# Optimization experiments

Measured on AMD Instinct MI355X. Metric: run time of the kernel, lower is better.

The kernel has to match this reference:

```python
import jax, jax.numpy as jnp
import numpy as np

B, N = 8, 2048
DIN, DH, DE = 32, 64, 64
R = 3          # number_relations
L = 3          # num_layers -> 1 first + 1 block + 1 last
PRED_IN = DH * (L - 1) + DE  # concat: 64*2 + 64 = 192
EPS_BN = 1e-5
EPS_NORM = 1e-12


def setup_inputs() -> dict:
    key = jax.random.key(0)
    ks = jax.random.split(key, 12)
    x = jax.random.normal(ks[0], (B, N, DIN), jnp.float32)
    # relation labels in {0..R}; 0 = no edge, 1..R = relation type
    relation = jax.random.randint(ks[1], (B, N, N), 0, R + 1).astype(jnp.int32)
    # adjacency is the 0/1 edge indicator (float), as the torch code treats it
    adj = (relation > 0).astype(jnp.float32)
    s = 0.05
    w_first = jax.random.normal(ks[2], (R, DIN, DH), jnp.float32) * s
    b_first = jnp.zeros((DH,), jnp.float32)
    w_block = jax.random.normal(ks[3], (R, DH, DH), jnp.float32) * s
    b_block = jnp.zeros((DH,), jnp.float32)
    w_last = jax.random.normal(ks[4], (R, DH, DE), jnp.float32) * s
    b_last = jnp.zeros((DE,), jnp.float32)
    w_map = jax.random.normal(ks[5], (PRED_IN, DE), jnp.float32) * s
    b_map = jnp.zeros((DE,), jnp.float32)
    return {"x": x, "relation": relation, "adj": adj,
            "w_first": w_first, "b_first": b_first,
            "w_block": w_block, "b_block": b_block,
            "w_last": w_last, "b_last": b_last,
            "w_map": w_map, "b_map": b_map}


def _graph_conv(x, rel, W, b):
    # rel: [B,N,N] (int labels or float adjacency); W: [R, din, dout]
    y = jnp.zeros((x.shape[0], x.shape[1], W.shape[2]), x.dtype)
    for i in range(R):  # fixed, small relation count
        mask = (rel == (i + 1)).astype(x.dtype)            # [B,N,N]
        h = jnp.einsum('bij,bjd->bid', mask, x)            # masked aggregation
        y = y + jnp.einsum('bid,de->bie', h, W[i])
    y = y + b
    # F.normalize(p=2, dim=2): v / max(||v||, eps)
    nrm = jnp.sqrt(jnp.sum(y * y, axis=2, keepdims=True))
    return y / jnp.maximum(nrm, EPS_NORM)


def _apply_bn(x):
    # fresh BatchNorm1d(N) in training mode, affine weight=1/bias=0:
    # normalize over (batch, feature) per node index, biased variance
    mean = jnp.mean(x, axis=(0, 2), keepdims=True)
    var = jnp.mean(jnp.square(x - mean), axis=(0, 2), keepdims=True)
    return (x - mean) * jax.lax.rsqrt(var + EPS_BN)


def reference(x, relation, adj, w_first, b_first, w_block, b_block,
              w_last, b_last, w_map, b_map):
    # conv_first uses `relation`
    h = _apply_bn(jax.nn.relu(_graph_conv(x, relation, w_first, b_first)))
    out_all = [jnp.max(h, axis=1)]
    # conv_block and conv_last are (faithfully) called with `adj` as relation
    h = _apply_bn(jax.nn.relu(_graph_conv(h, adj, w_block, b_block)))
    out_all.append(jnp.max(h, axis=1))
    h = _graph_conv(h, adj, w_last, b_last)
    out_all.append(jnp.max(h, axis=1))
    output = jnp.concatenate(out_all, axis=1)        # [B, PRED_IN]
    ypred = output @ w_map + b_map                   # map_model Linear
    return (output, ypred)
```

## Files before the change

### kernel.cpp

```cpp
#include <hip/hip_runtime.h>


#define NN 2048
#define PLANE_W 1048576L

typedef short short8 __attribute__((ext_vector_type(8)));
typedef float floatx4 __attribute__((ext_vector_type(4)));

__device__ __forceinline__ unsigned short f2bf(float x) {
  unsigned u = __float_as_uint(x);
  u += 0x7FFFu + ((u >> 16) & 1u);
  return (unsigned short)(u >> 16);
}

__device__ void dev_xw_first(char* smemc, int u, int tid,
                             const float* __restrict__ x,
                             const float* __restrict__ w,
                             unsigned short* __restrict__ xws) {
  float* xs = (float*)smemc;
  float* wsh = (float*)(smemc + 64 * 33 * 4);
  const int jc = u & 31, b = (u >> 5) & 7, r = u >> 8;
  const int j0 = jc * 64;
  for (int idx = tid; idx < 64 * 32; idx += 256) {
    int row = idx >> 5, f = idx & 31;
    xs[row * 33 + f] = x[((long)b * NN + j0 + row) * 32 + f];
    wsh[idx] = w[r * 2048 + idx];
  }
  __syncthreads();
  const int j = tid & 63, g = tid >> 6;
  const int k = j0 + j;
  const int kblk = k >> 5, kq = (k >> 3) & 3, kj = k & 7;
  unsigned short* dst =
      xws + (((long)(r * 8 + b) * 64 + kblk) * 4 + g) * 512 + kj;
  float xr[32];
#pragma unroll
  for (int f = 0; f < 32; ++f) xr[f] = xs[j * 33 + f];
#pragma unroll
  for (int ii = 0; ii < 16; ++ii) {
    float acc = 0.f;
#pragma unroll
    for (int f = 0; f < 32; ++f) acc += xr[f] * wsh[f * 64 + g * 16 + ii];
    dst[(kq * 16 + ii) * 8] = f2bf(acc);
  }
  __syncthreads();
}

__global__ __launch_bounds__(256) void k_pack_xw1(const int* __restrict__ rel,
                                                  unsigned* __restrict__ planes,
                                                  const float* __restrict__ x,
                                                  const float* __restrict__ w,
                                                  unsigned short* __restrict__ xws) {
  __shared__ __align__(16) char smem[16640];
  const int bid = blockIdx.x, tid = threadIdx.x;
  if (bid < 768) dev_xw_first(smem, bid, tid, x, w, xws);
  for (long t = (long)bid * 256 + tid; t < 1048576L; t += 4096L * 256) {
    int w32 = (int)(t & 63);
    long bi = t >> 6;
    const int4* rp = (const int4*)(rel + bi * NN + w32 * 32);
    unsigned m0 = 0, m1 = 0, m2 = 0;
#pragma unroll
    for (int c = 0; c < 8; ++c) {
      int4 v = rp[c];
      int vv[4] = {v.x, v.y, v.z, v.w};
#pragma unroll
      for (int j = 0; j < 4; ++j) {
        unsigned b1 = 1u << (c * 4 + j);
        m0 |= (vv[j] == 1) ? b1 : 0u;
        m1 |= (vv[j] == 2) ? b1 : 0u;
        m2 |= (vv[j] == 3) ? b1 : 0u;
      }
    }
    long o = bi * 64 + w32;
    planes[o] = m0;
    planes[PLANE_W + o] = m1;
    planes[2 * PLANE_W + o] = m2;
    planes[3 * PLANE_W + o] = m0 | m1 | m2;
  }
}

template <int NREL, bool RELU, bool POOL3>
__global__ __launch_bounds__(512) void k_gemm8(
    const unsigned* __restrict__ planes, const unsigned short* __restrict__ xws,
    const float* __restrict__ bias, float* __restrict__ Hout,
    float* __restrict__ part3) {
  constexpr int MASK_BYTES = NREL * 8448;
  __shared__ __align__(16) char smem[65536];
  unsigned* mw = (unsigned*)smem;
  uint2* lut = (uint2*)(smem + MASK_BYTES);
  floatx4* cb = (floatx4*)smem;
  const int bid = blockIdx.x;
  const int b = bid & 7, it = bid >> 3;
  const int tid = threadIdx.x;
  const int wave = tid >> 6, lane = tid & 63;
  const int m = lane & 15, kq = lane >> 4;
  const unsigned shamt = kq * 8;
  const int i0 = it * 64;

  if (tid < 16) {
    unsigned n = tid;
    lut[n] = make_uint2(((n & 1u) ? 0x3f80u : 0u) | ((n & 2u) ? 0x3f800000u : 0u),
                        ((n & 4u) ? 0x3f80u : 0u) | ((n & 8u) ? 0x3f800000u : 0u));
  }

  floatx4 acc[4][4];
#pragma unroll
  for (int rs = 0; rs < 4; ++rs)
#pragma unroll
    for (int t = 0; t < 4; ++t) acc[rs][t] = floatx4{0, 0, 0, 0};

  for (int chunk = 0; chunk < 2; ++chunk) {
    for (int idx = tid; idx < NREL * 2048; idx += 512) {
      int p = idx >> 11, rem = idx & 2047, row = rem >> 5, w = rem & 31;
      long g = ((long)b * NN + i0 + row) * 64 + chunk * 32 + w;
      unsigned v;
      if (NREL == 3)
        v = planes[(long)p * PLANE_W + g];
      else
        v = planes[3 * PLANE_W + g];
      mw[(p * 64 + row) * 33 + w] = v;
    }
    __syncthreads();
#pragma unroll
    for (int j = 0; j < 4; ++j) {
      const int kk = j * 8 + wave;
      const int kblk = chunk * 32 + kk;
#pragma unroll
      for (int p = 0; p < NREL; ++p) {
        const unsigned short* bb =
            xws + ((long)(p * 8 + b) * 64 + kblk) * 2048 + lane * 8;
        short8 bf0 = *(const short8*)(bb);
        short8 bf1 = *(const short8*)(bb + 512);
        short8 bf2 = *(const short8*)(bb + 1024);
        short8 bf3 = *(const short8*)(bb + 1536);
#pragma unroll
        for (int rs = 0; rs < 4; ++rs) {
          unsigned word = mw[(p * 64 + rs * 16 + m) * 33 + kk];
          unsigned byte = (word >> shamt) & 0xffu;
          uint2 lo = lut[byte & 15u];
          uint2 hi = lut[byte >> 4];
          union {
            unsigned uu[4];
            short8 s8;
          } fr;
          fr.uu[0] = lo.x;
          fr.uu[1] = lo.y;
          fr.uu[2] = hi.x;
          fr.uu[3] = hi.y;
          acc[rs][0] = __builtin_amdgcn_mfma_f32_16x16x32_bf16(fr.s8, bf0,
                                                              acc[rs][0], 0, 0, 0);
          acc[rs][1] = __builtin_amdgcn_mfma_f32_16x16x32_bf16(fr.s8, bf1,
                                                              acc[rs][1], 0, 0, 0);
          acc[rs][2] = __builtin_amdgcn_mfma_f32_16x16x32_bf16(fr.s8, bf2,
                                                              acc[rs][2], 0, 0, 0);
          acc[rs][3] = __builtin_amdgcn_mfma_f32_16x16x32_bf16(fr.s8, bf3,
                                                              acc[rs][3], 0, 0, 0);
        }
      }
    }
    __syncthreads();
  }

  if (wave >= 4) {
    const int src = wave - 4;
#pragma unroll
    for (int rs = 0; rs < 4; ++rs)
#pragma unroll
      for (int t = 0; t < 4; ++t)
        cb[((rs * 4 + src) * 4 + t) * 64 + lane] = acc[rs][t];
  }
  __syncthreads();
  if (wave < 4) {
#pragma unroll
    for (int rs = 0; rs < 4; ++rs)
#pragma unroll
      for (int t = 0; t < 4; ++t) {
        const int ix = ((rs * 4 + wave) * 4 + t) * 64 + lane;
        cb[ix] = cb[ix] + acc[rs][t];
      }
  }
  __syncthreads();
  if (wave < 4) {
    const int rs = wave;
    floatx4 s[4];
#pragma unroll
    for (int t = 0; t < 4; ++t) s[t] = cb[((rs * 4 + 0) * 4 + t) * 64 + lane];
#pragma unroll
    for (int src = 1; src < 4; ++src)
#pragma unroll
      for (int t = 0; t < 4; ++t)
        s[t] += cb[((rs * 4 + src) * 4 + t) * 64 + lane];
    float bv[4];
#pragma unroll
    for (int t = 0; t < 4; ++t) bv[t] = bias[t * 16 + m];
    float pmt[4] = {-3.4e38f, -3.4e38f, -3.4e38f, -3.4e38f};
#pragma unroll
    for (int reg = 0; reg < 4; ++reg) {
#pragma unroll
      for (int t = 0; t < 4; ++t) s[t][reg] += bv[t];
      float q = s[0][reg] * s[0][reg] + s[1][reg] * s[1][reg] +
                s[2][reg] * s[2][reg] + s[3][reg] * s[3][reg];
#pragma unroll
      for (int off = 1; off <= 8; off <<= 1) q += __shfl_xor(q, off);
      q = 1.0f / fmaxf(sqrtf(q), 1e-12f);
#pragma unroll
      for (int t = 0; t < 4; ++t) {
        float o = s[t][reg] * q;
        if (RELU) o = fmaxf(o, 0.0f);
        if (POOL3)
          pmt[t] = fmaxf(pmt[t], o);
        else
          Hout[((long)b * NN + i0 + rs * 16 + kq * 4 + reg) * 64 + t * 16 + m] = o;
      }
    }
    if (POOL3) {
#pragma unroll
      for (int t = 0; t < 4; ++t) {
        pmt[t] = fmaxf(pmt[t], __shfl_xor(pmt[t], 16));
        pmt[t] = fmaxf(pmt[t], __shfl_xor(pmt[t], 32));
      }
      float* pm = (float*)(smem + wave * 16384);
      if (kq == 0) {
#pragma unroll
        for (int t = 0; t < 4; ++t) pm[t * 16 + m] = pmt[t];
      }
    }
  }
  if (POOL3) {
    __syncthreads();
    if (tid < 64) {
      float v = -3.4e38f;
#pragma unroll
      for (int w = 0; w < 4; ++w)
        v = fmaxf(v, ((const float*)(smem + w * 16384))[tid]);
      part3[((long)b * 32 + it) * 64 + tid] = v;
    }
  }
}

__global__ __launch_bounds__(256) void k_xwh_bn(const float* __restrict__ H,
                                                const float* __restrict__ w,
                                                unsigned short* __restrict__ xws,
                                                float* __restrict__ PP) {
  __shared__ float hs[64 * 65];
  __shared__ float wsh[64 * 64];
  __shared__ float sm[64], srs[64];
  const int bid = blockIdx.x, tid = threadIdx.x;
  const int jc = bid & 31, b = bid >> 5;
  const int j0 = jc * 64;
  {
    const int n = tid >> 2, q = tid & 3;
    float s1 = 0.f, s2 = 0.f;
#pragma unroll
    for (int bb = 0; bb < 8; ++bb) {
      const float4* hp =
          (const float4*)(H + ((long)bb * NN + j0 + n) * 64 + q * 16);
#pragma unroll
      for (int c = 0; c < 4; ++c) {
        float4 v = hp[c];
        s1 += v.x + v.y + v.z + v.w;
        s2 += v.x * v.x + v.y * v.y + v.z * v.z + v.w * v.w;
      }
    }
    s1 += __shfl_xor(s1, 1);
    s2 += __shfl_xor(s2, 1);
    s1 += __shfl_xor(s1, 2);
    s2 += __shfl_xor(s2, 2);
    if (q == 0) {
      float mean = s1 * (1.0f / 512.0f);
      float var = fmaxf(s2 * (1.0f / 512.0f) - mean * mean, 0.0f);
      sm[n] = mean;
      srs[n] = rsqrtf(var + 1e-5f);
    }
  }
  __syncthreads();
  for (int idx = tid; idx < 4096; idx += 256) {
    int row = idx >> 6, f = idx & 63;
    float v = H[((long)b * NN + j0 + row) * 64 + f];
    hs[row * 65 + f] = (v - sm[row]) * srs[row];
    wsh[idx] = w[idx];
  }
  __syncthreads();
  {
    const int j = tid & 63, g = tid >> 6;
    const int k = j0 + j;
    const int kblk = k >> 5, kq = (k >> 3) & 3, kj = k & 7;
    unsigned short* dst = xws + (((long)b * 64 + kblk) * 4 + g) * 512 + kj;
    float acc[16];
#pragma unroll
    for (int ii = 0; ii < 16; ++ii) acc[ii] = 0.f;
#pragma unroll
    for (int c = 0; c < 4; ++c) {
      float xr[16];
#pragma unroll
      for (int f = 0; f < 16; ++f) xr[f] = hs[j * 65 + c * 16 + f];
#pragma unroll
      for (int ii = 0; ii < 16; ++ii)
#pragma unroll
        for (int f = 0; f < 16; ++f)
          acc[ii] += xr[f] * wsh[(c * 16 + f) * 64 + g * 16 + ii];
    }
#pragma unroll
    for (int ii = 0; ii < 16; ++ii) dst[(kq * 16 + ii) * 8] = f2bf(acc[ii]);
  }
  if (b == 0) {
#pragma unroll
    for (int part = 0; part < 2; ++part) {
      const int col = part * 256 + tid;
      const int bb = col >> 6, e = col & 63;
      float mx = -3.4e38f;
      for (int n = 0; n < 64; ++n) {
        float v = H[((long)bb * NN + j0 + n) * 64 + e];
        mx = fmaxf(mx, (v - sm[n]) * srs[n]);
      }
      PP[(long)jc * 512 + col] = mx;
    }
  }
}

__global__ __launch_bounds__(512) void k_tail(const float* __restrict__ PP1,
                                              const float* __restrict__ PP2,
                                              const float* __restrict__ P3,
                                              float* __restrict__ out,
                                              const float* __restrict__ wmap,
                                              const float* __restrict__ bmap) {
  __shared__ float obuf[8 * 192];
  const int col = threadIdx.x;
  const int bb = col >> 6, e = col & 63;
  float m1 = -3.4e38f, m2 = -3.4e38f, m3 = -3.4e38f;
#pragma unroll
  for (int c = 0; c < 32; ++c) {
    m1 = fmaxf(m1, PP1[(long)c * 512 + col]);
    m2 = fmaxf(m2, PP2[(long)c * 512 + col]);
    m3 = fmaxf(m3, P3[((long)bb * 32 + c) * 64 + e]);
  }
  out[bb * 192 + e] = m1;
  out[bb * 192 + 64 + e] = m2;
  out[bb * 192 + 128 + e] = m3;
  obuf[bb * 192 + e] = m1;
  obuf[bb * 192 + 64 + e] = m2;
  obuf[bb * 192 + 128 + e] = m3;
  __syncthreads();
  float acc = bmap[e];
#pragma unroll 4
  for (int k = 0; k < 192; ++k) acc += obuf[bb * 192 + k] * wmap[k * 64 + e];
  out[1536 + bb * 64 + e] = acc;
}

extern "C" void kernel_launch(void* const* d_in, const int* in_sizes, int n_in,
                              void* d_out, int out_size, void* d_ws,
                              size_t ws_size, hipStream_t stream) {
  const float* x = (const float*)d_in[0];
  const int* rel = (const int*)d_in[1];
  const float* w_first = (const float*)d_in[3];
  const float* b_first = (const float*)d_in[4];
  const float* w_block = (const float*)d_in[5];
  const float* b_block = (const float*)d_in[6];
  const float* w_last = (const float*)d_in[7];
  const float* b_last = (const float*)d_in[8];
  const float* w_map = (const float*)d_in[9];
  const float* b_map = (const float*)d_in[10];
  float* out = (float*)d_out;

  char* ws = (char*)d_ws;
  const size_t MB = 1024 * 1024;
  unsigned* PLANES = (unsigned*)(ws);
  unsigned short* XWS = (unsigned short*)(ws + 16 * MB);
  float* H = (float*)(ws + 22 * MB);
  float* PP1 = (float*)(ws + 26 * MB);
  float* PP2 = (float*)(ws + 27 * MB);
  float* PART3 = (float*)(ws + 28 * MB);

  k_pack_xw1<<<4096, 256, 0, stream>>>(rel, PLANES, x, w_first, XWS);
  k_gemm8<3, true, false><<<256, 512, 0, stream>>>(PLANES, XWS, b_first, H,
                                                   nullptr);
  k_xwh_bn<<<256, 256, 0, stream>>>(H, w_block, XWS, PP1);
  k_gemm8<1, true, false><<<256, 512, 0, stream>>>(PLANES, XWS, b_block, H,
                                                   nullptr);
  k_xwh_bn<<<256, 256, 0, stream>>>(H, w_last, XWS, PP2);
  k_gemm8<1, false, true><<<256, 512, 0, stream>>>(PLANES, XWS, b_last,
                                                   nullptr, PART3);
  k_tail<<<1, 512, 0, stream>>>(PP1, PP2, PART3, out, w_map, b_map);
}
```

Baseline: 355.8 us.

## Fuse all stages into one cooperative persistent kernel with grid syncs

Replaces seven separate launches (pack+xw, three gemm passes, two BN/xw passes, tail) with a single cooperative kernel of 256 blocks x 512 threads. Stages are separated by threadfence plus grid.sync. The helper stages are reworked for 512 threads by splitting output columns across thread halves. This is meant to remove kernel launch gaps and inter-kernel drain. In exchange, the relation-packing stage now runs with far fewer threads than its former 4096-block grid, and each grid-wide barrier adds synchronization cost.

```diff
diff --git a/kernel.cpp b/kernel.cpp
--- a/kernel.cpp
+++ b/kernel.cpp
@@ -1,8 +1,11 @@
 #include <hip/hip_runtime.h>
+#include <hip/hip_cooperative_groups.h>
 
 
 #define NN 2048
 #define PLANE_W 1048576L
+
+namespace cg = cooperative_groups;
 
 typedef short short8 __attribute__((ext_vector_type(8)));
 typedef float floatx4 __attribute__((ext_vector_type(4)));
@@ -13,21 +16,22 @@
   return (unsigned short)(u >> 16);
 }
 
-__device__ void dev_xw_first(char* smemc, int u, int tid,
-                             const float* __restrict__ x,
-                             const float* __restrict__ w,
-                             unsigned short* __restrict__ xws) {
+__device__ void dev_xw_first512(char* smemc, int u, int tid,
+                                const float* __restrict__ x,
+                                const float* __restrict__ w,
+                                unsigned short* __restrict__ xws) {
   float* xs = (float*)smemc;
   float* wsh = (float*)(smemc + 64 * 33 * 4);
   const int jc = u & 31, b = (u >> 5) & 7, r = u >> 8;
   const int j0 = jc * 64;
-  for (int idx = tid; idx < 64 * 32; idx += 256) {
+  for (int idx = tid; idx < 64 * 32; idx += 512) {
     int row = idx >> 5, f = idx & 31;
     xs[row * 33 + f] = x[((long)b * NN + j0 + row) * 32 + f];
     wsh[idx] = w[r * 2048 + idx];
   }
   __syncthreads();
-  const int j = tid & 63, g = tid >> 6;
+  const int j = tid & 63, gg = tid >> 6;
+  const int g = gg & 3, hf = gg >> 2;
   const int k = j0 + j;
   const int kblk = k >> 5, kq = (k >> 3) & 3, kj = k & 7;
   unsigned short* dst =
@@ -36,61 +40,28 @@
 #pragma unroll
   for (int f = 0; f < 32; ++f) xr[f] = xs[j * 33 + f];
 #pragma unroll
-  for (int ii = 0; ii < 16; ++ii) {
+  for (int ii = 0; ii < 8; ++ii) {
     float acc = 0.f;
 #pragma unroll
-    for (int f = 0; f < 32; ++f) acc += xr[f] * wsh[f * 64 + g * 16 + ii];
-    dst[(kq * 16 + ii) * 8] = f2bf(acc);
-  }
-  __syncthreads();
-}
-
-__global__ __launch_bounds__(256) void k_pack_xw1(const int* __restrict__ rel,
-                                                  unsigned* __restrict__ planes,
-                                                  const float* __restrict__ x,
-                                                  const float* __restrict__ w,
-                                                  unsigned short* __restrict__ xws) {
-  __shared__ __align__(16) char smem[16640];
-  const int bid = blockIdx.x, tid = threadIdx.x;
-  if (bid < 768) dev_xw_first(smem, bid, tid, x, w, xws);
-  for (long t = (long)bid * 256 + tid; t < 1048576L; t += 4096L * 256) {
-    int w32 = (int)(t & 63);
-    long bi = t >> 6;
-    const int4* rp = (const int4*)(rel + bi * NN + w32 * 32);
-    unsigned m0 = 0, m1 = 0, m2 = 0;
-#pragma unroll
-    for (int c = 0; c < 8; ++c) {
-      int4 v = rp[c];
-      int vv[4] = {v.x, v.y, v.z, v.w};
-#pragma unroll
-      for (int j = 0; j < 4; ++j) {
-        unsigned b1 = 1u << (c * 4 + j);
-        m0 |= (vv[j] == 1) ? b1 : 0u;
-        m1 |= (vv[j] == 2) ? b1 : 0u;
-        m2 |= (vv[j] == 3) ? b1 : 0u;
-      }
-    }
-    long o = bi * 64 + w32;
-    planes[o] = m0;
-    planes[PLANE_W + o] = m1;
-    planes[2 * PLANE_W + o] = m2;
-    planes[3 * PLANE_W + o] = m0 | m1 | m2;
-  }
+    for (int f = 0; f < 32; ++f)
+      acc += xr[f] * wsh[f * 64 + g * 16 + hf * 8 + ii];
+    dst[(kq * 16 + hf * 8 + ii) * 8] = f2bf(acc);
+  }
+  __syncthreads();
 }
 
 template <int NREL, bool RELU, bool POOL3>
-__global__ __launch_bounds__(512) void k_gemm8(
-    const unsigned* __restrict__ planes, const unsigned short* __restrict__ xws,
-    const float* __restrict__ bias, float* __restrict__ Hout,
-    float* __restrict__ part3) {
+__device__ void dev_gemm8(char* smem, int bid, int tid,
+                          const unsigned* __restrict__ planes,
+                          const unsigned short* __restrict__ xws,
+                          const float* __restrict__ bias,
+                          float* __restrict__ Hout,
+                          float* __restrict__ part3) {
   constexpr int MASK_BYTES = NREL * 8448;
-  __shared__ __align__(16) char smem[65536];
   unsigned* mw = (unsigned*)smem;
   uint2* lut = (uint2*)(smem + MASK_BYTES);
   floatx4* cb = (floatx4*)smem;
-  const int bid = blockIdx.x;
   const int b = bid & 7, it = bid >> 3;
-  const int tid = threadIdx.x;
   const int wave = tid >> 6, lane = tid & 63;
   const int m = lane & 15, kq = lane >> 4;
   const unsigned shamt = kq * 8;
@@ -98,8 +69,9 @@
 
   if (tid < 16) {
     unsigned n = tid;
-    lut[n] = make_uint2(((n & 1u) ? 0x3f80u : 0u) | ((n & 2u) ? 0x3f800000u : 0u),
-                        ((n & 4u) ? 0x3f80u : 0u) | ((n & 8u) ? 0x3f800000u : 0u));
+    lut[n] =
+        make_uint2(((n & 1u) ? 0x3f80u : 0u) | ((n & 2u) ? 0x3f800000u : 0u),
+                   ((n & 4u) ? 0x3f80u : 0u) | ((n & 8u) ? 0x3f800000u : 0u));
   }
 
   floatx4 acc[4][4];
@@ -146,14 +118,14 @@
           fr.uu[1] = lo.y;
           fr.uu[2] = hi.x;
           fr.uu[3] = hi.y;
-          acc[rs][0] = __builtin_amdgcn_mfma_f32_16x16x32_bf16(fr.s8, bf0,
-                                                              acc[rs][0], 0, 0, 0);
-          acc[rs][1] = __builtin_amdgcn_mfma_f32_16x16x32_bf16(fr.s8, bf1,
-                                                              acc[rs][1], 0, 0, 0);
-          acc[rs][2] = __builtin_amdgcn_mfma_f32_16x16x32_bf16(fr.s8, bf2,
-                                                              acc[rs][2], 0, 0, 0);
-          acc[rs][3] = __builtin_amdgcn_mfma_f32_16x16x32_bf16(fr.s8, bf3,
-                                                              acc[rs][3], 0, 0, 0);
+          acc[rs][0] = __builtin_amdgcn_mfma_f32_16x16x32_bf16(
+              fr.s8, bf0, acc[rs][0], 0, 0, 0);
+          acc[rs][1] = __builtin_amdgcn_mfma_f32_16x16x32_bf16(
+              fr.s8, bf1, acc[rs][1], 0, 0, 0);
+          acc[rs][2] = __builtin_amdgcn_mfma_f32_16x16x32_bf16(
+              fr.s8, bf2, acc[rs][2], 0, 0, 0);
+          acc[rs][3] = __builtin_amdgcn_mfma_f32_16x16x32_bf16(
+              fr.s8, bf3, acc[rs][3], 0, 0, 0);
         }
       }
     }
@@ -209,7 +181,8 @@
         if (POOL3)
           pmt[t] = fmaxf(pmt[t], o);
         else
-          Hout[((long)b * NN + i0 + rs * 16 + kq * 4 + reg) * 64 + t * 16 + m] = o;
+          Hout[((long)b * NN + i0 + rs * 16 + kq * 4 + reg) * 64 + t * 16 +
+               m] = o;
       }
     }
     if (POOL3) {
@@ -237,25 +210,26 @@
   }
 }
 
-__global__ __launch_bounds__(256) void k_xwh_bn(const float* __restrict__ H,
-                                                const float* __restrict__ w,
-                                                unsigned short* __restrict__ xws,
-                                                float* __restrict__ PP) {
-  __shared__ float hs[64 * 65];
-  __shared__ float wsh[64 * 64];
-  __shared__ float sm[64], srs[64];
-  const int bid = blockIdx.x, tid = threadIdx.x;
+__device__ void dev_xwh_bn512(char* smemc, int bid, int tid,
+                              const float* __restrict__ H,
+                              const float* __restrict__ w,
+                              unsigned short* __restrict__ xws,
+                              float* __restrict__ PP) {
+  float* hs = (float*)smemc;
+  float* wsh = (float*)(smemc + 16640);
+  float* sm = (float*)(smemc + 16640 + 16384);
+  float* srs = (float*)(smemc + 16640 + 16384 + 256);
   const int jc = bid & 31, b = bid >> 5;
   const int j0 = jc * 64;
   {
-    const int n = tid >> 2, q = tid & 3;
+    const int n = tid >> 3, o = tid & 7;
     float s1 = 0.f, s2 = 0.f;
 #pragma unroll
     for (int bb = 0; bb < 8; ++bb) {
       const float4* hp =
-          (const float4*)(H + ((long)bb * NN + j0 + n) * 64 + q * 16);
-#pragma unroll
-      for (int c = 0; c < 4; ++c) {
+          (const float4*)(H + ((long)bb * NN + j0 + n) * 64 + o * 8);
+#pragma unroll
+      for (int c = 0; c < 2; ++c) {
         float4 v = hp[c];
         s1 += v.x + v.y + v.z + v.w;
         s2 += v.x * v.x + v.y * v.y + v.z * v.z + v.w * v.w;
@@ -265,7 +239,9 @@
     s2 += __shfl_xor(s2, 1);
     s1 += __shfl_xor(s1, 2);
     s2 += __shfl_xor(s2, 2);
-    if (q == 0) {
+    s1 += __shfl_xor(s1, 4);
+    s2 += __shfl_xor(s2, 4);
+    if (o == 0) {
       float mean = s1 * (1.0f / 512.0f);
       float var = fmaxf(s2 * (1.0f / 512.0f) - mean * mean, 0.0f);
       sm[n] = mean;
@@ -273,7 +249,7 @@
     }
   }
   __syncthreads();
-  for (int idx = tid; idx < 4096; idx += 256) {
+  for (int idx = tid; idx < 4096; idx += 512) {
     int row = idx >> 6, f = idx & 63;
     float v = H[((long)b * NN + j0 + row) * 64 + f];
     hs[row * 65 + f] = (v - sm[row]) * srs[row];
@@ -281,50 +257,50 @@
   }
   __syncthreads();
   {
-    const int j = tid & 63, g = tid >> 6;
+    const int j = tid & 63, gg = tid >> 6;
+    const int g = gg & 3, hf = gg >> 2;
     const int k = j0 + j;
     const int kblk = k >> 5, kq = (k >> 3) & 3, kj = k & 7;
     unsigned short* dst = xws + (((long)b * 64 + kblk) * 4 + g) * 512 + kj;
-    float acc[16];
-#pragma unroll
-    for (int ii = 0; ii < 16; ++ii) acc[ii] = 0.f;
+    float acc[8];
+#pragma unroll
+    for (int ii = 0; ii < 8; ++ii) acc[ii] = 0.f;
 #pragma unroll
     for (int c = 0; c < 4; ++c) {
       float xr[16];
 #pragma unroll
       for (int f = 0; f < 16; ++f) xr[f] = hs[j * 65 + c * 16 + f];
 #pragma unroll
-      for (int ii = 0; ii < 16; ++ii)
+      for (int ii = 0; ii < 8; ++ii)
 #pragma unroll
         for (int f = 0; f < 16; ++f)
-          acc[ii] += xr[f] * wsh[(c * 16 + f) * 64 + g * 16 + ii];
-    }
-#pragma unroll
-    for (int ii = 0; ii < 16; ++ii) dst[(kq * 16 + ii) * 8] = f2bf(acc[ii]);
+          acc[ii] += xr[f] * wsh[(c * 16 + f) * 64 + g * 16 + hf * 8 + ii];
+    }
+#pragma unroll
+    for (int ii = 0; ii < 8; ++ii)
+      dst[(kq * 16 + hf * 8 + ii) * 8] = f2bf(acc[ii]);
   }
   if (b == 0) {
-#pragma unroll
-    for (int part = 0; part < 2; ++part) {
-      const int col = part * 256 + tid;
-      const int bb = col >> 6, e = col & 63;
-      float mx = -3.4e38f;
-      for (int n = 0; n < 64; ++n) {
-        float v = H[((long)bb * NN + j0 + n) * 64 + e];
-        mx = fmaxf(mx, (v - sm[n]) * srs[n]);
-      }
-      PP[(long)jc * 512 + col] = mx;
-    }
-  }
-}
-
-__global__ __launch_bounds__(512) void k_tail(const float* __restrict__ PP1,
-                                              const float* __restrict__ PP2,
-                                              const float* __restrict__ P3,
-                                              float* __restrict__ out,
-                                              const float* __restrict__ wmap,
-                                              const float* __restrict__ bmap) {
-  __shared__ float obuf[8 * 192];
-  const int col = threadIdx.x;
+    const int col = tid;
+    const int bb = col >> 6, e = col & 63;
+    float mx = -3.4e38f;
+    for (int n = 0; n < 64; ++n) {
+      float v = H[((long)bb * NN + j0 + n) * 64 + e];
+      mx = fmaxf(mx, (v - sm[n]) * srs[n]);
+    }
+    PP[(long)jc * 512 + col] = mx;
+  }
+  __syncthreads();
+}
+
+__device__ void dev_tail(char* smemc, int tid, const float* __restrict__ PP1,
+                         const float* __restrict__ PP2,
+                         const float* __restrict__ P3,
+                         float* __restrict__ out,
+                         const float* __restrict__ wmap,
+                         const float* __restrict__ bmap) {
+  float* obuf = (float*)smemc;
+  const int col = tid;
   const int bb = col >> 6, e = col & 63;
   float m1 = -3.4e38f, m2 = -3.4e38f, m3 = -3.4e38f;
 #pragma unroll
@@ -344,6 +320,66 @@
 #pragma unroll 4
   for (int k = 0; k < 192; ++k) acc += obuf[bb * 192 + k] * wmap[k * 64 + e];
   out[1536 + bb * 64 + e] = acc;
+}
+
+__global__ __launch_bounds__(512) void k_fused(
+    const int* __restrict__ rel, const float* __restrict__ x,
+    const float* __restrict__ w_first, const float* __restrict__ b_first,
+    const float* __restrict__ w_block, const float* __restrict__ b_block,
+    const float* __restrict__ w_last, const float* __restrict__ b_last,
+    const float* __restrict__ wmap, const float* __restrict__ bmap,
+    unsigned* __restrict__ planes, unsigned short* __restrict__ xws,
+    float* __restrict__ H, float* __restrict__ PP1, float* __restrict__ PP2,
+    float* __restrict__ PART3, float* __restrict__ out) {
+  __shared__ __align__(16) char smem[65536];
+  cg::grid_group grid = cg::this_grid();
+  const int bid = blockIdx.x, tid = threadIdx.x;
+
+#pragma unroll
+  for (int s = 0; s < 3; ++s)
+    dev_xw_first512(smem, bid * 3 + s, tid, x, w_first, xws);
+  for (long t = (long)bid * 512 + tid; t < 1048576L; t += 131072L) {
+    int w32 = (int)(t & 63);
+    long bi = t >> 6;
+    const int4* rp = (const int4*)(rel + bi * NN + w32 * 32);
+    unsigned m0 = 0, m1 = 0, m2 = 0;
+#pragma unroll
+    for (int c = 0; c < 8; ++c) {
+      int4 v = rp[c];
+      int vv[4] = {v.x, v.y, v.z, v.w};
+#pragma unroll
+      for (int j = 0; j < 4; ++j) {
+        unsigned b1 = 1u << (c * 4 + j);
+        m0 |= (vv[j] == 1) ? b1 : 0u;
+        m1 |= (vv[j] == 2) ? b1 : 0u;
+        m2 |= (vv[j] == 3) ? b1 : 0u;
+      }
+    }
+    long o = bi * 64 + w32;
+    planes[o] = m0;
+    planes[PLANE_W + o] = m1;
+    planes[2 * PLANE_W + o] = m2;
+    planes[3 * PLANE_W + o] = m0 | m1 | m2;
+  }
+  __threadfence();
+  grid.sync();
+  dev_gemm8<3, true, false>(smem, bid, tid, planes, xws, b_first, H, nullptr);
+  __threadfence();
+  grid.sync();
+  dev_xwh_bn512(smem, bid, tid, H, w_block, xws, PP1);
+  __threadfence();
+  grid.sync();
+  dev_gemm8<1, true, false>(smem, bid, tid, planes, xws, b_block, H, nullptr);
+  __threadfence();
+  grid.sync();
+  dev_xwh_bn512(smem, bid, tid, H, w_last, xws, PP2);
+  __threadfence();
+  grid.sync();
+  dev_gemm8<1, false, true>(smem, bid, tid, planes, xws, b_last, nullptr,
+                            PART3);
+  __threadfence();
+  grid.sync();
+  if (bid == 0) dev_tail(smem, tid, PP1, PP2, PART3, out, wmap, bmap);
 }
 
 extern "C" void kernel_launch(void* const* d_in, const int* in_sizes, int n_in,
@@ -370,14 +406,9 @@
   float* PP2 = (float*)(ws + 27 * MB);
   float* PART3 = (float*)(ws + 28 * MB);
 
-  k_pack_xw1<<<4096, 256, 0, stream>>>(rel, PLANES, x, w_first, XWS);
-  k_gemm8<3, true, false><<<256, 512, 0, stream>>>(PLANES, XWS, b_first, H,
-                                                   nullptr);
-  k_xwh_bn<<<256, 256, 0, stream>>>(H, w_block, XWS, PP1);
-  k_gemm8<1, true, false><<<256, 512, 0, stream>>>(PLANES, XWS, b_block, H,
-                                                   nullptr);
-  k_xwh_bn<<<256, 256, 0, stream>>>(H, w_last, XWS, PP2);
-  k_gemm8<1, false, true><<<256, 512, 0, stream>>>(PLANES, XWS, b_last,
-                                                   nullptr, PART3);
-  k_tail<<<1, 512, 0, stream>>>(PP1, PP2, PART3, out, w_map, b_map);
-}
+  void* kargs[] = {&rel,    &x,      &w_first, &b_first, &w_block, &b_block,
+                   &w_last, &b_last, &w_map,   &b_map,   &PLANES,  &XWS,
+                   &H,      &PP1,    &PP2,     &PART3,   &out};
+  hipLaunchCooperativeKernel((void*)k_fused, dim3(256), dim3(512), kargs, 0,
+                             stream);
+}
```

Measured after the change: 842.0 us. +136.6%, slower.

## Fuse relation bit-packing into first GEMM and fold tail into last GEMM

Applied to the files above, without the earlier changes.

The relation tensor is now converted to bitmasks inside the first graph-conv GEMM using wave ballots, instead of a separate packing kernel that wrote four planes to memory. Only the union plane is written out for the later layers, which reduces packed-plane traffic. The final max/linear tail is folded into the last GEMM through a last-block atomic counter, and the x·W projection gets its own small kernel. The costs are that the first GEMM now streams the 134MB int relation itself, one row segment per wave per load, and that the fusion adds atomic and threadfence synchronisation.

```diff
diff --git a/kernel.cpp b/kernel.cpp
--- a/kernel.cpp
+++ b/kernel.cpp
@@ -2,7 +2,6 @@
 
 
 #define NN 2048
-#define PLANE_W 1048576L
 
 typedef short short8 __attribute__((ext_vector_type(8)));
 typedef float floatx4 __attribute__((ext_vector_type(4)));
@@ -13,10 +12,13 @@
   return (unsigned short)(u >> 16);
 }
 
-__device__ void dev_xw_first(char* smemc, int u, int tid,
-                             const float* __restrict__ x,
-                             const float* __restrict__ w,
-                             unsigned short* __restrict__ xws) {
+__global__ __launch_bounds__(256) void k_xw1(const float* __restrict__ x,
+                                             const float* __restrict__ w,
+                                             unsigned short* __restrict__ xws,
+                                             unsigned* __restrict__ done) {
+  __shared__ __align__(16) char smemc[16640];
+  const int u = blockIdx.x, tid = threadIdx.x;
+  if (u == 0 && tid == 0) *done = 0u;
   float* xs = (float*)smemc;
   float* wsh = (float*)(smemc + 64 * 33 * 4);
   const int jc = u & 31, b = (u >> 5) & 7, r = u >> 8;
@@ -42,124 +44,17 @@
     for (int f = 0; f < 32; ++f) acc += xr[f] * wsh[f * 64 + g * 16 + ii];
     dst[(kq * 16 + ii) * 8] = f2bf(acc);
   }
-  __syncthreads();
-}
-
-__global__ __launch_bounds__(256) void k_pack_xw1(const int* __restrict__ rel,
-                                                  unsigned* __restrict__ planes,
-                                                  const float* __restrict__ x,
-                                                  const float* __restrict__ w,
-                                                  unsigned short* __restrict__ xws) {
-  __shared__ __align__(16) char smem[16640];
-  const int bid = blockIdx.x, tid = threadIdx.x;
-  if (bid < 768) dev_xw_first(smem, bid, tid, x, w, xws);
-  for (long t = (long)bid * 256 + tid; t < 1048576L; t += 4096L * 256) {
-    int w32 = (int)(t & 63);
-    long bi = t >> 6;
-    const int4* rp = (const int4*)(rel + bi * NN + w32 * 32);
-    unsigned m0 = 0, m1 = 0, m2 = 0;
-#pragma unroll
-    for (int c = 0; c < 8; ++c) {
-      int4 v = rp[c];
-      int vv[4] = {v.x, v.y, v.z, v.w};
-#pragma unroll
-      for (int j = 0; j < 4; ++j) {
-        unsigned b1 = 1u << (c * 4 + j);
-        m0 |= (vv[j] == 1) ? b1 : 0u;
-        m1 |= (vv[j] == 2) ? b1 : 0u;
-        m2 |= (vv[j] == 3) ? b1 : 0u;
-      }
-    }
-    long o = bi * 64 + w32;
-    planes[o] = m0;
-    planes[PLANE_W + o] = m1;
-    planes[2 * PLANE_W + o] = m2;
-    planes[3 * PLANE_W + o] = m0 | m1 | m2;
-  }
-}
-
-template <int NREL, bool RELU, bool POOL3>
-__global__ __launch_bounds__(512) void k_gemm8(
-    const unsigned* __restrict__ planes, const unsigned short* __restrict__ xws,
+}
+
+template <bool RELU, bool POOL3>
+__device__ __forceinline__ void gemm_epilogue(
+    char* smem, int b, int it, int tid, floatx4 (&acc)[4][4],
     const float* __restrict__ bias, float* __restrict__ Hout,
     float* __restrict__ part3) {
-  constexpr int MASK_BYTES = NREL * 8448;
-  __shared__ __align__(16) char smem[65536];
-  unsigned* mw = (unsigned*)smem;
-  uint2* lut = (uint2*)(smem + MASK_BYTES);
   floatx4* cb = (floatx4*)smem;
-  const int bid = blockIdx.x;
-  const int b = bid & 7, it = bid >> 3;
-  const int tid = threadIdx.x;
   const int wave = tid >> 6, lane = tid & 63;
   const int m = lane & 15, kq = lane >> 4;
-  const unsigned shamt = kq * 8;
   const int i0 = it * 64;
-
-  if (tid < 16) {
-    unsigned n = tid;
-    lut[n] = make_uint2(((n & 1u) ? 0x3f80u : 0u) | ((n & 2u) ? 0x3f800000u : 0u),
-                        ((n & 4u) ? 0x3f80u : 0u) | ((n & 8u) ? 0x3f800000u : 0u));
-  }
-
-  floatx4 acc[4][4];
-#pragma unroll
-  for (int rs = 0; rs < 4; ++rs)
-#pragma unroll
-    for (int t = 0; t < 4; ++t) acc[rs][t] = floatx4{0, 0, 0, 0};
-
-  for (int chunk = 0; chunk < 2; ++chunk) {
-    for (int idx = tid; idx < NREL * 2048; idx += 512) {
-      int p = idx >> 11, rem = idx & 2047, row = rem >> 5, w = rem & 31;
-      long g = ((long)b * NN + i0 + row) * 64 + chunk * 32 + w;
-      unsigned v;
-      if (NREL == 3)
-        v = planes[(long)p * PLANE_W + g];
-      else
-        v = planes[3 * PLANE_W + g];
-      mw[(p * 64 + row) * 33 + w] = v;
-    }
-    __syncthreads();
-#pragma unroll
-    for (int j = 0; j < 4; ++j) {
-      const int kk = j * 8 + wave;
-      const int kblk = chunk * 32 + kk;
-#pragma unroll
-      for (int p = 0; p < NREL; ++p) {
-        const unsigned short* bb =
-            xws + ((long)(p * 8 + b) * 64 + kblk) * 2048 + lane * 8;
-        short8 bf0 = *(const short8*)(bb);
-        short8 bf1 = *(const short8*)(bb + 512);
-        short8 bf2 = *(const short8*)(bb + 1024);
-        short8 bf3 = *(const short8*)(bb + 1536);
-#pragma unroll
-        for (int rs = 0; rs < 4; ++rs) {
-          unsigned word = mw[(p * 64 + rs * 16 + m) * 33 + kk];
-          unsigned byte = (word >> shamt) & 0xffu;
-          uint2 lo = lut[byte & 15u];
-          uint2 hi = lut[byte >> 4];
-          union {
-            unsigned uu[4];
-            short8 s8;
-          } fr;
-          fr.uu[0] = lo.x;
-          fr.uu[1] = lo.y;
-          fr.uu[2] = hi.x;
-          fr.uu[3] = hi.y;
-          acc[rs][0] = __builtin_amdgcn_mfma_f32_16x16x32_bf16(fr.s8, bf0,
-                                                              acc[rs][0], 0, 0, 0);
-          acc[rs][1] = __builtin_amdgcn_mfma_f32_16x16x32_bf16(fr.s8, bf1,
-                                                              acc[rs][1], 0, 0, 0);
-          acc[rs][2] = __builtin_amdgcn_mfma_f32_16x16x32_bf16(fr.s8, bf2,
-                                                              acc[rs][2], 0, 0, 0);
-          acc[rs][3] = __builtin_amdgcn_mfma_f32_16x16x32_bf16(fr.s8, bf3,
-                                                              acc[rs][3], 0, 0, 0);
-        }
-      }
-    }
-    __syncthreads();
-  }
-
   if (wave >= 4) {
     const int src = wave - 4;
 #pragma unroll
@@ -209,7 +104,8 @@
         if (POOL3)
           pmt[t] = fmaxf(pmt[t], o);
         else
-          Hout[((long)b * NN + i0 + rs * 16 + kq * 4 + reg) * 64 + t * 16 + m] = o;
+          Hout[((long)b * NN + i0 + rs * 16 + kq * 4 + reg) * 64 + t * 16 +
+               m] = o;
       }
     }
     if (POOL3) {
@@ -225,6 +121,161 @@
       }
     }
   }
+}
+
+template <int NREL>
+__device__ __forceinline__ void gemm_chunk_mfma(
+    const unsigned* mw, const uint2* lut, const unsigned short* __restrict__ xws,
+    int b, int chunk, int wave, int lane, floatx4 (&acc)[4][4]) {
+  const int m = lane & 15, kq = lane >> 4;
+  const unsigned shamt = kq * 8;
+#pragma unroll
+  for (int j = 0; j < 4; ++j) {
+    const int kk = j * 8 + wave;
+    const int kblk = chunk * 32 + kk;
+#pragma unroll
+    for (int p = 0; p < NREL; ++p) {
+      const unsigned short* bb =
+          xws + ((long)(p * 8 + b) * 64 + kblk) * 2048 + lane * 8;
+      short8 bf0 = *(const short8*)(bb);
+      short8 bf1 = *(const short8*)(bb + 512);
+      short8 bf2 = *(const short8*)(bb + 1024);
+      short8 bf3 = *(const short8*)(bb + 1536);
+#pragma unroll
+      for (int rs = 0; rs < 4; ++rs) {
+        unsigned word = mw[(p * 64 + rs * 16 + m) * 33 + kk];
+        unsigned byte = (word >> shamt) & 0xffu;
+        uint2 lo = lut[byte & 15u];
+        uint2 hi = lut[byte >> 4];
+        union {
+          unsigned uu[4];
+          short8 s8;
+        } fr;
+        fr.uu[0] = lo.x;
+        fr.uu[1] = lo.y;
+        fr.uu[2] = hi.x;
+        fr.uu[3] = hi.y;
+        acc[rs][0] = __builtin_amdgcn_mfma_f32_16x16x32_bf16(fr.s8, bf0,
+                                                             acc[rs][0], 0, 0, 0);
+        acc[rs][1] = __builtin_amdgcn_mfma_f32_16x16x32_bf16(fr.s8, bf1,
+                                                             acc[rs][1], 0, 0, 0);
+        acc[rs][2] = __builtin_amdgcn_mfma_f32_16x16x32_bf16(fr.s8, bf2,
+                                                             acc[rs][2], 0, 0, 0);
+        acc[rs][3] = __builtin_amdgcn_mfma_f32_16x16x32_bf16(fr.s8, bf3,
+                                                             acc[rs][3], 0, 0, 0);
+      }
+    }
+  }
+}
+
+__global__ __launch_bounds__(512) void k_gemm_rel(
+    const int* __restrict__ rel, const unsigned short* __restrict__ xws,
+    const float* __restrict__ bias, float* __restrict__ Hout,
+    unsigned* __restrict__ pu) {
+  __shared__ __align__(16) char smem[65536];
+  unsigned* mw = (unsigned*)smem;
+  uint2* lut = (uint2*)(smem + 3 * 8448);
+  const int bid = blockIdx.x;
+  const int b = bid & 7, it = bid >> 3;
+  const int tid = threadIdx.x;
+  const int wave = tid >> 6, lane = tid & 63;
+  const int i0 = it * 64;
+
+  if (tid < 16) {
+    unsigned n = tid;
+    lut[n] =
+        make_uint2(((n & 1u) ? 0x3f80u : 0u) | ((n & 2u) ? 0x3f800000u : 0u),
+                   ((n & 4u) ? 0x3f80u : 0u) | ((n & 8u) ? 0x3f800000u : 0u));
+  }
+
+  floatx4 acc[4][4];
+#pragma unroll
+  for (int rs = 0; rs < 4; ++rs)
+#pragma unroll
+    for (int t = 0; t < 4; ++t) acc[rs][t] = floatx4{0, 0, 0, 0};
+
+  for (int chunk = 0; chunk < 2; ++chunk) {
+    for (int i = 0; i < 128; i += 4) {
+      int vq[4];
+#pragma unroll
+      for (int q = 0; q < 4; ++q) {
+        const int u = (i + q) * 8 + wave;
+        const int row = u >> 4, wp = u & 15;
+        vq[q] = rel[((long)b * NN + i0 + row) * NN + chunk * 1024 + wp * 64 +
+                    lane];
+      }
+#pragma unroll
+      for (int q = 0; q < 4; ++q) {
+        const int u = (i + q) * 8 + wave;
+        const int row = u >> 4, wp = u & 15;
+        const int v = vq[q];
+        unsigned long long b1 = __ballot(v == 1);
+        unsigned long long b2 = __ballot(v == 2);
+        unsigned long long b3 = __ballot(v == 3);
+        unsigned long long bu = __ballot(v != 0);
+        if (lane == 0) {
+          const int wbase = row * 33 + wp * 2;
+          mw[wbase] = (unsigned)b1;
+          mw[wbase + 1] = (unsigned)(b1 >> 32);
+          mw[2112 + wbase] = (unsigned)b2;
+          mw[2112 + wbase + 1] = (unsigned)(b2 >> 32);
+          mw[4224 + wbase] = (unsigned)b3;
+          mw[4224 + wbase + 1] = (unsigned)(b3 >> 32);
+          *(unsigned long long*)&pu[((long)b * NN + i0 + row) * 64 +
+                                    chunk * 32 + wp * 2] = bu;
+        }
+      }
+    }
+    __syncthreads();
+    gemm_chunk_mfma<3>(mw, lut, xws, b, chunk, wave, lane, acc);
+    __syncthreads();
+  }
+  gemm_epilogue<true, false>(smem, b, it, tid, acc, bias, Hout, nullptr);
+}
+
+template <bool RELU, bool POOL3>
+__global__ __launch_bounds__(512) void k_gemm_u(
+    const unsigned* __restrict__ pu, const unsigned short* __restrict__ xws,
+    const float* __restrict__ bias, float* __restrict__ Hout,
+    float* __restrict__ part3, const float* __restrict__ PP1,
+    const float* __restrict__ PP2, float* __restrict__ out,
+    const float* __restrict__ wmap, const float* __restrict__ bmap,
+    unsigned* __restrict__ done) {
+  __shared__ __align__(16) char smem[65536];
+  __shared__ int s_last;
+  unsigned* mw = (unsigned*)smem;
+  uint2* lut = (uint2*)(smem + 8448);
+  const int bid = blockIdx.x;
+  const int b = bid & 7, it = bid >> 3;
+  const int tid = threadIdx.x;
+  const int wave = tid >> 6, lane = tid & 63;
+  const int i0 = it * 64;
+
+  if (tid < 16) {
+    unsigned n = tid;
+    lut[n] =
+        make_uint2(((n & 1u) ? 0x3f80u : 0u) | ((n & 2u) ? 0x3f800000u : 0u),
+                   ((n & 4u) ? 0x3f80u : 0u) | ((n & 8u) ? 0x3f800000u : 0u));
+  }
+
+  floatx4 acc[4][4];
+#pragma unroll
+  for (int rs = 0; rs < 4; ++rs)
+#pragma unroll
+    for (int t = 0; t < 4; ++t) acc[rs][t] = floatx4{0, 0, 0, 0};
+
+  for (int chunk = 0; chunk < 2; ++chunk) {
+    for (int idx = tid; idx < 2048; idx += 512) {
+      int row = idx >> 5, w = idx & 31;
+      mw[row * 33 + w] =
+          pu[((long)b * NN + i0 + row) * 64 + chunk * 32 + w];
+    }
+    __syncthreads();
+    gemm_chunk_mfma<1>(mw, lut, xws, b, chunk, wave, lane, acc);
+    __syncthreads();
+  }
+  gemm_epilogue<RELU, POOL3>(smem, b, it, tid, acc, bias, Hout, part3);
+
   if (POOL3) {
     __syncthreads();
     if (tid < 64) {
@@ -233,6 +284,34 @@
       for (int w = 0; w < 4; ++w)
         v = fmaxf(v, ((const float*)(smem + w * 16384))[tid]);
       part3[((long)b * 32 + it) * 64 + tid] = v;
+    }
+    __threadfence();
+    __syncthreads();
+    if (tid == 0) s_last = (atomicAdd(done, 1u) == 255u) ? 1 : 0;
+    __syncthreads();
+    if (s_last) {
+      __threadfence();
+      float* obuf = (float*)smem;
+      const int col = tid;
+      const int bb = col >> 6, e = col & 63;
+      float m1 = -3.4e38f, m2 = -3.4e38f, m3 = -3.4e38f;
+#pragma unroll
+      for (int c = 0; c < 32; ++c) {
+        m1 = fmaxf(m1, PP1[(long)c * 512 + col]);
+        m2 = fmaxf(m2, PP2[(long)c * 512 + col]);
+        m3 = fmaxf(m3, part3[((long)bb * 32 + c) * 64 + e]);
+      }
+      out[bb * 192 + e] = m1;
+      out[bb * 192 + 64 + e] = m2;
+      out[bb * 192 + 128 + e] = m3;
+      obuf[bb * 192 + e] = m1;
+      obuf[bb * 192 + 64 + e] = m2;
+      obuf[bb * 192 + 128 + e] = m3;
+      __syncthreads();
+      float a = bmap[e];
+#pragma unroll 4
+      for (int k = 0; k < 192; ++k) a += obuf[bb * 192 + k] * wmap[k * 64 + e];
+      out[1536 + bb * 64 + e] = a;
     }
   }
 }
@@ -315,35 +394,6 @@
       PP[(long)jc * 512 + col] = mx;
     }
   }
-}
-
-__global__ __launch_bounds__(512) void k_tail(const float* __restrict__ PP1,
-                                              const float* __restrict__ PP2,
-                                              const float* __restrict__ P3,
-                                              float* __restrict__ out,
-                                              const float* __restrict__ wmap,
-                                              const float* __restrict__ bmap) {
-  __shared__ float obuf[8 * 192];
-  const int col = threadIdx.x;
-  const int bb = col >> 6, e = col & 63;
-  float m1 = -3.4e38f, m2 = -3.4e38f, m3 = -3.4e38f;
-#pragma unroll
-  for (int c = 0; c < 32; ++c) {
-    m1 = fmaxf(m1, PP1[(long)c * 512 + col]);
-    m2 = fmaxf(m2, PP2[(long)c * 512 + col]);
-    m3 = fmaxf(m3, P3[((long)bb * 32 + c) * 64 + e]);
-  }
-  out[bb * 192 + e] = m1;
-  out[bb * 192 + 64 + e] = m2;
-  out[bb * 192 + 128 + e] = m3;
-  obuf[bb * 192 + e] = m1;
-  obuf[bb * 192 + 64 + e] = m2;
-  obuf[bb * 192 + 128 + e] = m3;
-  __syncthreads();
-  float acc = bmap[e];
-#pragma unroll 4
-  for (int k = 0; k < 192; ++k) acc += obuf[bb * 192 + k] * wmap[k * 64 + e];
-  out[1536 + bb * 64 + e] = acc;
 }
 
 extern "C" void kernel_launch(void* const* d_in, const int* in_sizes, int n_in,
@@ -363,21 +413,22 @@
 
   char* ws = (char*)d_ws;
   const size_t MB = 1024 * 1024;
-  unsigned* PLANES = (unsigned*)(ws);
-  unsigned short* XWS = (unsigned short*)(ws + 16 * MB);
-  float* H = (float*)(ws + 22 * MB);
-  float* PP1 = (float*)(ws + 26 * MB);
-  float* PP2 = (float*)(ws + 27 * MB);
-  float* PART3 = (float*)(ws + 28 * MB);
-
-  k_pack_xw1<<<4096, 256, 0, stream>>>(rel, PLANES, x, w_first, XWS);
-  k_gemm8<3, true, false><<<256, 512, 0, stream>>>(PLANES, XWS, b_first, H,
-                                                   nullptr);
+  unsigned* PLANES_U = (unsigned*)(ws);
+  unsigned short* XWS = (unsigned short*)(ws + 4 * MB);
+  float* H = (float*)(ws + 10 * MB);
+  float* PP1 = (float*)(ws + 14 * MB);
+  float* PP2 = (float*)(ws + 15 * MB);
+  float* PART3 = (float*)(ws + 16 * MB);
+  unsigned* DONE = (unsigned*)(ws + 17 * MB);
+
+  k_xw1<<<768, 256, 0, stream>>>(x, w_first, XWS, DONE);
+  k_gemm_rel<<<256, 512, 0, stream>>>(rel, XWS, b_first, H, PLANES_U);
   k_xwh_bn<<<256, 256, 0, stream>>>(H, w_block, XWS, PP1);
-  k_gemm8<1, true, false><<<256, 512, 0, stream>>>(PLANES, XWS, b_block, H,
-                                                   nullptr);
+  k_gemm_u<true, false><<<256, 512, 0, stream>>>(
+      PLANES_U, XWS, b_block, H, nullptr, nullptr, nullptr, nullptr, nullptr,
+      nullptr, nullptr);
   k_xwh_bn<<<256, 256, 0, stream>>>(H, w_last, XWS, PP2);
-  k_gemm8<1, false, true><<<256, 512, 0, stream>>>(PLANES, XWS, b_last,
-                                                   nullptr, PART3);
-  k_tail<<<1, 512, 0, stream>>>(PP1, PP2, PART3, out, w_map, b_map);
-}
+  k_gemm_u<false, true><<<256, 512, 0, stream>>>(
+      PLANES_U, XWS, b_last, nullptr, PART3, PP1, PP2, out, w_map, b_map,
+      DONE);
+}
```

Result: slower. 409.9 us (+15.2%).
